# Kernel optimization log

Hardware: AMD Instinct MI355X
Metric: run time of the kernel (lower is better)

Reference implementation:

```python
import jax, jax.numpy as jnp
import numpy as np

N_HEAD = 8
DIM_K = 64
DIM_MODEL = N_HEAD * DIM_K  # 512; must equal seq_len for the final batch_dot
SCALE = DIM_K ** 0.5


def setup_inputs() -> dict:
    key = jax.random.key(0)
    ks = jax.random.split(key, 4)
    B, S, D_IN = 32, 512, 128
    x = jax.random.normal(ks[0], (B, S, D_IN), dtype=jnp.float32)
    init = 0.02
    Wq = jax.random.normal(ks[1], (D_IN * N_HEAD, DIM_MODEL), dtype=jnp.float32) * init
    Wk = jax.random.normal(ks[2], (D_IN * N_HEAD, DIM_MODEL), dtype=jnp.float32) * init
    Wv = jax.random.normal(ks[3], (D_IN * N_HEAD, DIM_MODEL), dtype=jnp.float32) * init
    z = jnp.zeros((DIM_MODEL,), dtype=jnp.float32)
    return {"x": x, "Wq": Wq, "bq": z, "Wk": Wk, "bk": z, "Wv": Wv, "bv": z}


def reference(x, Wq, bq, Wk, bk, Wv, bv):
    # Tile input n_head times along feature dim (matches K.concatenate([q]*n_head))
    xt = jnp.concatenate([x] * N_HEAD, axis=-1)          # [B, S, d_in*n_head]
    q = xt @ Wq + bq                                      # [B, S, dim_model]
    k = xt @ Wk + bk
    v = xt @ Wv + bv
    # K.batch_dot(q, k, axes=[-1,-1]) -> q @ k^T per batch
    scores = jnp.einsum('bsd,btd->bst', q, k) / SCALE     # [B, S, S]
    attn = jax.nn.softmax(scores, axis=-1)
    # K.batch_dot(v, attn, axes=[2,-1]): out[b,i,j] = sum_k v[b,i,k]*attn[b,j,k]
    # (only valid because S == dim_model, as in the original buggy layer)
    out = jnp.einsum('bik,bjk->bij', v, attn)             # [B, S, S]
    return out
```

## Files before the change

kernel.cpp:

```cpp
#include <hip/hip_runtime.h>


typedef unsigned short u16;
typedef __attribute__((ext_vector_type(8))) short bf16x8;
typedef __attribute__((ext_vector_type(4))) float f32x4;
typedef __attribute__((ext_vector_type(2))) float f32x2;

__device__ inline u16 f2bf(float f) {
  unsigned u = __float_as_uint(f);
  u = u + 0x7fffu + ((u >> 16) & 1u);
  return (u16)(u >> 16);
}
__device__ inline float bf2f(u16 h) { return __uint_as_float(((unsigned)h) << 16); }

__device__ inline void gl16(const u16* g, u16* l) {
  __builtin_amdgcn_global_load_lds(
      (const __attribute__((address_space(1))) unsigned int*)g,
      (__attribute__((address_space(3))) unsigned int*)l, 16, 0, 0);
}

__global__ __launch_bounds__(256)
void prep_w(const float* __restrict__ Wq, const float* __restrict__ Wk,
            const float* __restrict__ Wv,
            u16* __restrict__ WTh, u16* __restrict__ WTl) {
  __shared__ float sm[128][17];
  int t  = blockIdx.x >> 5;
  int nb = blockIdx.x & 31;
  const float* W = (t == 0) ? Wq : (t == 1) ? Wk : Wv;
  int n0 = nb << 4;
  int nl = threadIdx.x & 15;
  int kq = threadIdx.x >> 4;
  float s[8];
#pragma unroll
  for (int i = 0; i < 8; ++i) s[i] = 0.f;
#pragma unroll
  for (int h = 0; h < 8; ++h)
#pragma unroll
    for (int i = 0; i < 8; ++i)
      s[i] += W[(h * 128 + kq + (i << 4)) * 512 + n0 + nl];
#pragma unroll
  for (int i = 0; i < 8; ++i) sm[kq + (i << 4)][nl] = s[i];
  __syncthreads();
  int no = threadIdx.x >> 4;
  int k8 = (threadIdx.x & 15) << 3;
  bf16x8 h8, l8;
#pragma unroll
  for (int c = 0; c < 8; ++c) {
    float v = sm[k8 + c][no];
    u16 h = f2bf(v);
    h8[c] = (short)h;
    l8[c] = (short)f2bf(v - bf2f(h));
  }
  long o = (long)t * 65536 + (long)(n0 + no) * 128 + k8;
  *(bf16x8*)&WTh[o] = h8;
  *(bf16x8*)&WTl[o] = l8;
}

__global__ __launch_bounds__(256)
void split_x(const float* __restrict__ x, u16* __restrict__ xh, u16* __restrict__ xl) {
  int i = blockIdx.x * 256 + threadIdx.x;
  const f32x4* xx = (const f32x4*)x;
  f32x4 a = xx[i * 2], b = xx[i * 2 + 1];
  float v[8] = {a[0], a[1], a[2], a[3], b[0], b[1], b[2], b[3]};
  bf16x8 h8, l8;
#pragma unroll
  for (int j = 0; j < 8; ++j) {
    u16 h = f2bf(v[j]);
    h8[j] = (short)h;
    l8[j] = (short)f2bf(v[j] - bf2f(h));
  }
  ((bf16x8*)xh)[i] = h8;
  ((bf16x8*)xl)[i] = l8;
}

__global__ __launch_bounds__(256, 2)
void proj_fused(const u16* __restrict__ xh, const u16* __restrict__ xl,
                const u16* __restrict__ WTh, const u16* __restrict__ WTl,
                u16* __restrict__ Qh, u16* __restrict__ Kh, u16* __restrict__ Vh,
                const float* __restrict__ bq, const float* __restrict__ bk,
                const float* __restrict__ bv) {
  __shared__ __align__(16) char ldsraw[65536];
  u16* st = (u16*)ldsraw;

  int tid = threadIdx.x;
  int bid = blockIdx.x;
  bid = (bid & 7) * 192 + (bid >> 3);
  int which = bid % 3;
  int tile  = bid / 3;
  int mt = tile >> 2;
  int nt = tile & 3;

  const u16* Ah = xh + (long)mt * (128 * 128);
  const u16* Al = xl + (long)mt * (128 * 128);
  const u16* Bh = WTh + which * 65536 + nt * 16384;
  const u16* Bl = WTl + which * 65536 + nt * 16384;
  const float* bias = (which == 0) ? bq : (which == 1) ? bk : bv;
  u16* C = (which == 0) ? Qh : (which == 1) ? Kh : Vh;

  int lane = tid & 63;
  int wv = tid >> 6;
  int wm = (wv >> 1) << 6;
  int wn = (wv & 1) << 6;
  int frow = lane & 15;
  int fk = (lane >> 4) << 3;

  f32x4 acc[4][4];
#pragma unroll
  for (int i = 0; i < 4; ++i)
#pragma unroll
    for (int j = 0; j < 4; ++j) {
      f32x4 z = {0.f, 0.f, 0.f, 0.f};
      acc[i][j] = z;
    }

  for (int kk = 0; kk < 2; ++kk) {
    int k0 = kk << 6;
#pragma unroll
    for (int j = 0; j < 4; ++j) {
      int c = j * 256 + tid;
      int row = c >> 3;
      int scol = ((c & 7) ^ (row & 7)) << 3;
      int ga = row * 128 + k0 + scol;
      int lo = c << 3;
      gl16(Ah + ga, st + lo);
      gl16(Al + ga, st + 8192 + lo);
      gl16(Bh + ga, st + 16384 + lo);
      gl16(Bl + ga, st + 24576 + lo);
    }
    __syncthreads();
#pragma unroll
    for (int ks = 0; ks < 2; ++ks) {
      int kb = (ks << 5) + fk;
      bf16x8 a_h[4], a_l[4], b_h[4], b_l[4];
#pragma unroll
      for (int i = 0; i < 4; ++i) {
        int ar = wm + (i << 4) + frow;
        int ao = ar * 64 + (kb ^ ((ar & 7) << 3));
        a_h[i] = *(const bf16x8*)&st[ao];
        a_l[i] = *(const bf16x8*)&st[8192 + ao];
        int br = wn + (i << 4) + frow;
        int bo = br * 64 + (kb ^ ((br & 7) << 3));
        b_h[i] = *(const bf16x8*)&st[16384 + bo];
        b_l[i] = *(const bf16x8*)&st[24576 + bo];
      }
#pragma unroll
      for (int i = 0; i < 4; ++i)
#pragma unroll
        for (int j = 0; j < 4; ++j) {
          acc[i][j] = __builtin_amdgcn_mfma_f32_16x16x32_bf16(a_h[i], b_h[j], acc[i][j], 0, 0, 0);
          acc[i][j] = __builtin_amdgcn_mfma_f32_16x16x32_bf16(a_l[i], b_h[j], acc[i][j], 0, 0, 0);
          acc[i][j] = __builtin_amdgcn_mfma_f32_16x16x32_bf16(a_h[i], b_l[j], acc[i][j], 0, 0, 0);
        }
    }
    __syncthreads();
  }

  float* tr = ((float*)ldsraw) + wv * 2112;
  int lr = lane >> 3;
  int c8 = (lane & 7) << 3;
  int colbase = (nt << 7) + wn + c8;
  float bb[8];
#pragma unroll
  for (int c = 0; c < 8; ++c) bb[c] = bias[colbase + c];
  long rowg0 = (long)(mt << 7) + wm;
#pragma unroll
  for (int q = 0; q < 2; ++q) {
#pragma unroll
    for (int il = 0; il < 2; ++il) {
      int i = (q << 1) + il;
#pragma unroll
      for (int j = 0; j < 4; ++j)
#pragma unroll
        for (int r = 0; r < 4; ++r)
          tr[((il << 4) + ((lane >> 4) << 2) + r) * 66 + (j << 4) + (lane & 15)] =
              acc[i][j][r];
    }
#pragma unroll
    for (int p = 0; p < 4; ++p) {
      int rr = (p << 3) + lr;
      float v[8];
      *(f32x2*)&v[0] = *(const f32x2*)&tr[rr * 66 + c8];
      *(f32x2*)&v[2] = *(const f32x2*)&tr[rr * 66 + c8 + 2];
      *(f32x2*)&v[4] = *(const f32x2*)&tr[rr * 66 + c8 + 4];
      *(f32x2*)&v[6] = *(const f32x2*)&tr[rr * 66 + c8 + 6];
      bf16x8 o8;
#pragma unroll
      for (int c = 0; c < 8; ++c) o8[c] = (short)f2bf(v[c] + bb[c]);
      *(bf16x8*)&C[(rowg0 + (q << 5) + rr) * 512 + colbase] = o8;
    }
  }
}

__global__ __launch_bounds__(256, 4)
void nt_gemm1(const u16* __restrict__ A, const u16* __restrict__ B,
              float* __restrict__ C, float scale) {
  __shared__ __align__(16) u16 lds[2][128 * 64];
  int tid = threadIdx.x;
  int bid = blockIdx.x;
  bid = (bid & 7) * 64 + (bid >> 3);
  int b  = bid >> 4;
  int t  = bid & 15;
  int mt = t >> 2;
  int nt = t & 3;
  const u16* pA = A + (long)b * 262144 + (long)mt * (128 * 512);
  const u16* pB = B + (long)b * 262144 + (long)nt * (128 * 512);

  int lane = tid & 63;
  int wv = tid >> 6;
  int wm = (wv >> 1) << 6;
  int wn = (wv & 1) << 6;
  int frow = lane & 15;
  int fk = (lane >> 4) << 3;

  f32x4 acc[4][4];
#pragma unroll
  for (int i = 0; i < 4; ++i)
#pragma unroll
    for (int j = 0; j < 4; ++j) {
      f32x4 z = {0.f, 0.f, 0.f, 0.f};
      acc[i][j] = z;
    }

  for (int kk = 0; kk < 8; ++kk) {
    int k0 = kk << 6;
#pragma unroll
    for (int j = 0; j < 4; ++j) {
      int c = j * 256 + tid;
      int row = c >> 3;
      int scol = ((c & 7) ^ (row & 7)) << 3;
      long g = (long)row * 512 + k0 + scol;
      int lo = c << 3;
      gl16(pA + g, &lds[0][lo]);
      gl16(pB + g, &lds[1][lo]);
    }
    __syncthreads();
#pragma unroll
    for (int ks = 0; ks < 2; ++ks) {
      int kb = (ks << 5) + fk;
      bf16x8 av[4], bv_[4];
#pragma unroll
      for (int i = 0; i < 4; ++i) {
        int ar = wm + (i << 4) + frow;
        av[i] = *(const bf16x8*)&lds[0][ar * 64 + (kb ^ ((ar & 7) << 3))];
        int br = wn + (i << 4) + frow;
        bv_[i] = *(const bf16x8*)&lds[1][br * 64 + (kb ^ ((br & 7) << 3))];
      }
#pragma unroll
      for (int i = 0; i < 4; ++i)
#pragma unroll
        for (int j = 0; j < 4; ++j)
          acc[i][j] = __builtin_amdgcn_mfma_f32_16x16x32_bf16(av[i], bv_[j], acc[i][j], 0, 0, 0);
    }
    __syncthreads();
  }

  int rbase = (mt << 7) + wm + ((lane >> 4) << 2);
  int cbase = (nt << 7) + wn + (lane & 15);
  float* Cb = C + (long)b * 262144;
#pragma unroll
  for (int i = 0; i < 4; ++i)
#pragma unroll
    for (int j = 0; j < 4; ++j)
#pragma unroll
      for (int r = 0; r < 4; ++r)
        Cb[(long)(rbase + (i << 4) + r) * 512 + cbase + (j << 4)] = acc[i][j][r] * scale;
}

__global__ __launch_bounds__(256)
void softmax_rows(const float* __restrict__ S, u16* __restrict__ Ah) {
  int row  = (blockIdx.x << 2) + (threadIdx.x >> 6);
  int lane = threadIdx.x & 63;
  long base = (long)row * 512;
  const f32x4* s4 = (const f32x4*)(S + base);
  float v[8];
  *(f32x4*)&v[0] = s4[lane * 2];
  *(f32x4*)&v[4] = s4[lane * 2 + 1];
  float m = v[0];
#pragma unroll
  for (int j = 1; j < 8; ++j) m = fmaxf(m, v[j]);
#pragma unroll
  for (int o = 32; o > 0; o >>= 1) m = fmaxf(m, __shfl_xor(m, o));
  float sum = 0.f;
#pragma unroll
  for (int j = 0; j < 8; ++j) { v[j] = __expf(v[j] - m); sum += v[j]; }
#pragma unroll
  for (int o = 32; o > 0; o >>= 1) sum += __shfl_xor(sum, o);
  float inv = 1.f / sum;
  bf16x8 o8;
#pragma unroll
  for (int j = 0; j < 8; ++j) o8[j] = (short)f2bf(v[j] * inv);
  *(bf16x8*)&Ah[base + lane * 8] = o8;
}

extern "C" void kernel_launch(void* const* d_in, const int* in_sizes, int n_in,
                              void* d_out, int out_size, void* d_ws, size_t ws_size,
                              hipStream_t stream) {
  const float* x  = (const float*)d_in[0];
  const float* Wq = (const float*)d_in[1];
  const float* bq = (const float*)d_in[2];
  const float* Wk = (const float*)d_in[3];
  const float* bk = (const float*)d_in[4];
  const float* Wv = (const float*)d_in[5];
  const float* bv = (const float*)d_in[6];
  float* out = (float*)d_out;

  char* ws = (char*)d_ws;
  size_t off = 0;
  auto alloc = [&](size_t bytes) -> char* {
    char* p = ws + off;
    off = (off + bytes + 255) & ~(size_t)255;
    return p;
  };
  u16* WTh = (u16*)alloc((size_t)3 * 512 * 128 * 2);
  u16* WTl = (u16*)alloc((size_t)3 * 512 * 128 * 2);
  u16* xh  = (u16*)alloc((size_t)16384 * 128 * 2);
  u16* xl  = (u16*)alloc((size_t)16384 * 128 * 2);
  u16* Qh  = (u16*)alloc((size_t)16384 * 512 * 2);
  u16* Kh  = (u16*)alloc((size_t)16384 * 512 * 2);
  u16* Vh  = (u16*)alloc((size_t)16384 * 512 * 2);
  float* sc = (float*)alloc((size_t)32 * 512 * 512 * 4);
  u16* ah = Qh;

  prep_w<<<96, 256, 0, stream>>>(Wq, Wk, Wv, WTh, WTl);
  split_x<<<1024, 256, 0, stream>>>(x, xh, xl);
  proj_fused<<<1536, 256, 0, stream>>>(xh, xl, WTh, WTl, Qh, Kh, Vh, bq, bk, bv);
  nt_gemm1<<<512, 256, 0, stream>>>(Qh, Kh, sc, 0.125f);
  softmax_rows<<<4096, 256, 0, stream>>>(sc, ah);
  nt_gemm1<<<512, 256, 0, stream>>>(Vh, ah, out, 1.f);
}
```

Measured before the change: 92.92 us.

## Fuse QK^T, softmax and V·attn^T into one attention kernel per 64-row block

Replaces the scores GEMM, the separate softmax kernel and the second GEMM with one kernel. Each 512-thread block computes a 64x512 score tile, does the row softmax in registers with LDS reductions, keeps the bf16 probabilities in LDS, then multiplies by V. This removes the fp32 score round trip through global memory (32 MB written and read) and two kernel launches. In exchange it uses 128 KB of LDS, so only one block fits per CU, and the grid is just 256 blocks. K and V are also reloaded by each of the 8 row blocks per batch.

```diff
diff --git a/kernel.cpp b/kernel.cpp
--- a/kernel.cpp
+++ b/kernel.cpp
@@ -191,105 +191,219 @@
   }
 }
 
-__global__ __launch_bounds__(256, 4)
-void nt_gemm1(const u16* __restrict__ A, const u16* __restrict__ B,
-              float* __restrict__ C, float scale) {
-  __shared__ __align__(16) u16 lds[2][128 * 64];
+__global__ __launch_bounds__(512, 1)
+void attn_fused(const u16* __restrict__ Q, const u16* __restrict__ K,
+                const u16* __restrict__ V, float* __restrict__ OUT) {
+  __shared__ __align__(16) char LDS[131072];
+  u16* ldsQ = (u16*)LDS;
+  u16* ldsK = (u16*)(LDS + 8192);
+  u16* ldsV = (u16*)(LDS + 65536);
+  float* smax = (float*)(LDS + 73728);
+  float* ssum = (float*)(LDS + 74752);
+
   int tid = threadIdx.x;
   int bid = blockIdx.x;
-  bid = (bid & 7) * 64 + (bid >> 3);
-  int b  = bid >> 4;
-  int t  = bid & 15;
-  int mt = t >> 2;
-  int nt = t & 3;
-  const u16* pA = A + (long)b * 262144 + (long)mt * (128 * 512);
-  const u16* pB = B + (long)b * 262144 + (long)nt * (128 * 512);
+  bid = (bid & 7) * 32 + (bid >> 3);
+  int b  = bid >> 3;
+  int jb = bid & 7;
+
+  const u16* Qp = Q + ((long)b * 512 + jb * 64) * 512;
+  const u16* Kp = K + (long)b * 262144;
+  const u16* Vp = V + (long)b * 262144;
 
   int lane = tid & 63;
-  int wv = tid >> 6;
-  int wm = (wv >> 1) << 6;
-  int wn = (wv & 1) << 6;
+  int wv   = tid >> 6;
   int frow = lane & 15;
-  int fk = (lane >> 4) << 3;
-
-  f32x4 acc[4][4];
-#pragma unroll
-  for (int i = 0; i < 4; ++i)
-#pragma unroll
-    for (int j = 0; j < 4; ++j) {
+  int hi4  = lane >> 4;
+  int fk   = hi4 << 3;
+
+  int wm1 = (wv >> 2) << 5;
+  int wn1 = (wv & 3) << 7;
+  f32x4 acc[2][8];
+#pragma unroll
+  for (int i = 0; i < 2; ++i)
+#pragma unroll
+    for (int j = 0; j < 8; ++j) {
       f32x4 z = {0.f, 0.f, 0.f, 0.f};
       acc[i][j] = z;
     }
 
+  int qrow = tid >> 3, qcc = tid & 7;
+  int qscol = (qcc ^ (qrow & 7)) << 3;
   for (int kk = 0; kk < 8; ++kk) {
     int k0 = kk << 6;
-#pragma unroll
-    for (int j = 0; j < 4; ++j) {
-      int c = j * 256 + tid;
-      int row = c >> 3;
-      int scol = ((c & 7) ^ (row & 7)) << 3;
-      long g = (long)row * 512 + k0 + scol;
-      int lo = c << 3;
-      gl16(pA + g, &lds[0][lo]);
-      gl16(pB + g, &lds[1][lo]);
+    gl16(Qp + qrow * 512 + k0 + qscol, ldsQ + tid * 8);
+#pragma unroll
+    for (int j = 0; j < 8; ++j) {
+      int c = (j << 9) + tid;
+      int row = c >> 3, cc = c & 7;
+      int scol = (cc ^ (row & 7)) << 3;
+      gl16(Kp + (long)row * 512 + k0 + scol, ldsK + c * 8);
     }
     __syncthreads();
 #pragma unroll
     for (int ks = 0; ks < 2; ++ks) {
       int kb = (ks << 5) + fk;
-      bf16x8 av[4], bv_[4];
-#pragma unroll
-      for (int i = 0; i < 4; ++i) {
-        int ar = wm + (i << 4) + frow;
-        av[i] = *(const bf16x8*)&lds[0][ar * 64 + (kb ^ ((ar & 7) << 3))];
-        int br = wn + (i << 4) + frow;
-        bv_[i] = *(const bf16x8*)&lds[1][br * 64 + (kb ^ ((br & 7) << 3))];
-      }
-#pragma unroll
-      for (int i = 0; i < 4; ++i)
-#pragma unroll
-        for (int j = 0; j < 4; ++j)
-          acc[i][j] = __builtin_amdgcn_mfma_f32_16x16x32_bf16(av[i], bv_[j], acc[i][j], 0, 0, 0);
-    }
-    __syncthreads();
-  }
-
-  int rbase = (mt << 7) + wm + ((lane >> 4) << 2);
-  int cbase = (nt << 7) + wn + (lane & 15);
-  float* Cb = C + (long)b * 262144;
-#pragma unroll
-  for (int i = 0; i < 4; ++i)
-#pragma unroll
-    for (int j = 0; j < 4; ++j)
+      bf16x8 a[2], bb[8];
+#pragma unroll
+      for (int i = 0; i < 2; ++i) {
+        int ar = wm1 + (i << 4) + frow;
+        a[i] = *(const bf16x8*)&ldsQ[ar * 64 + (kb ^ ((ar & 7) << 3))];
+      }
+#pragma unroll
+      for (int j = 0; j < 8; ++j) {
+        int br = wn1 + (j << 4) + frow;
+        bb[j] = *(const bf16x8*)&ldsK[br * 64 + (kb ^ ((br & 7) << 3))];
+      }
+#pragma unroll
+      for (int i = 0; i < 2; ++i)
+#pragma unroll
+        for (int j = 0; j < 8; ++j)
+          acc[i][j] = __builtin_amdgcn_mfma_f32_16x16x32_bf16(a[i], bb[j], acc[i][j], 0, 0, 0);
+    }
+    __syncthreads();
+  }
+
+  float mx[2][4];
+#pragma unroll
+  for (int i = 0; i < 2; ++i)
+#pragma unroll
+    for (int r = 0; r < 4; ++r) {
+      float m = acc[i][0][r];
+#pragma unroll
+      for (int j = 1; j < 8; ++j) m = fmaxf(m, acc[i][j][r]);
+      mx[i][r] = m;
+    }
+#pragma unroll
+  for (int msk = 1; msk < 16; msk <<= 1)
+#pragma unroll
+    for (int i = 0; i < 2; ++i)
 #pragma unroll
       for (int r = 0; r < 4; ++r)
-        Cb[(long)(rbase + (i << 4) + r) * 512 + cbase + (j << 4)] = acc[i][j][r] * scale;
-}
-
-__global__ __launch_bounds__(256)
-void softmax_rows(const float* __restrict__ S, u16* __restrict__ Ah) {
-  int row  = (blockIdx.x << 2) + (threadIdx.x >> 6);
-  int lane = threadIdx.x & 63;
-  long base = (long)row * 512;
-  const f32x4* s4 = (const f32x4*)(S + base);
-  float v[8];
-  *(f32x4*)&v[0] = s4[lane * 2];
-  *(f32x4*)&v[4] = s4[lane * 2 + 1];
-  float m = v[0];
-#pragma unroll
-  for (int j = 1; j < 8; ++j) m = fmaxf(m, v[j]);
-#pragma unroll
-  for (int o = 32; o > 0; o >>= 1) m = fmaxf(m, __shfl_xor(m, o));
-  float sum = 0.f;
-#pragma unroll
-  for (int j = 0; j < 8; ++j) { v[j] = __expf(v[j] - m); sum += v[j]; }
-#pragma unroll
-  for (int o = 32; o > 0; o >>= 1) sum += __shfl_xor(sum, o);
-  float inv = 1.f / sum;
-  bf16x8 o8;
-#pragma unroll
-  for (int j = 0; j < 8; ++j) o8[j] = (short)f2bf(v[j] * inv);
-  *(bf16x8*)&Ah[base + lane * 8] = o8;
+        mx[i][r] = fmaxf(mx[i][r], __shfl_xor(mx[i][r], msk));
+  if (frow == 0) {
+#pragma unroll
+    for (int i = 0; i < 2; ++i)
+#pragma unroll
+      for (int r = 0; r < 4; ++r)
+        smax[(wm1 + (i << 4) + (hi4 << 2) + r) * 4 + (wv & 3)] = mx[i][r];
+  }
+  __syncthreads();
+  float mf[2][4];
+#pragma unroll
+  for (int i = 0; i < 2; ++i)
+#pragma unroll
+    for (int r = 0; r < 4; ++r) {
+      f32x4 mv = *(const f32x4*)&smax[(wm1 + (i << 4) + (hi4 << 2) + r) * 4];
+      mf[i][r] = fmaxf(fmaxf(mv[0], mv[1]), fmaxf(mv[2], mv[3]));
+    }
+  float sm[2][4];
+#pragma unroll
+  for (int i = 0; i < 2; ++i)
+#pragma unroll
+    for (int r = 0; r < 4; ++r) sm[i][r] = 0.f;
+#pragma unroll
+  for (int i = 0; i < 2; ++i)
+#pragma unroll
+    for (int j = 0; j < 8; ++j)
+#pragma unroll
+      for (int r = 0; r < 4; ++r) {
+        float p = __expf((acc[i][j][r] - mf[i][r]) * 0.125f);
+        acc[i][j][r] = p;
+        sm[i][r] += p;
+      }
+#pragma unroll
+  for (int msk = 1; msk < 16; msk <<= 1)
+#pragma unroll
+    for (int i = 0; i < 2; ++i)
+#pragma unroll
+      for (int r = 0; r < 4; ++r)
+        sm[i][r] += __shfl_xor(sm[i][r], msk);
+  if (frow == 0) {
+#pragma unroll
+    for (int i = 0; i < 2; ++i)
+#pragma unroll
+      for (int r = 0; r < 4; ++r)
+        ssum[(wm1 + (i << 4) + (hi4 << 2) + r) * 4 + (wv & 3)] = sm[i][r];
+  }
+  __syncthreads();
+  float inv[2][4];
+#pragma unroll
+  for (int i = 0; i < 2; ++i)
+#pragma unroll
+    for (int r = 0; r < 4; ++r) {
+      f32x4 sv = *(const f32x4*)&ssum[(wm1 + (i << 4) + (hi4 << 2) + r) * 4];
+      inv[i][r] = 1.f / (sv[0] + sv[1] + sv[2] + sv[3]);
+    }
+#pragma unroll
+  for (int i = 0; i < 2; ++i)
+#pragma unroll
+    for (int j = 0; j < 8; ++j)
+#pragma unroll
+      for (int r = 0; r < 4; ++r) {
+        int row = wm1 + (i << 4) + (hi4 << 2) + r;
+        int col = wn1 + (j << 4) + frow;
+        int byt = ((row << 10) + (col << 1)) ^ ((row & 7) << 4);
+        *(u16*)(LDS + byt) = f2bf(acc[i][j][r] * inv[i][r]);
+      }
+  __syncthreads();
+
+  int wm2 = (wv >> 1) << 7;
+  int wn2 = (wv & 1) << 5;
+  f32x4 a2[8][2];
+#pragma unroll
+  for (int i = 0; i < 8; ++i)
+#pragma unroll
+    for (int j = 0; j < 2; ++j) {
+      f32x4 z = {0.f, 0.f, 0.f, 0.f};
+      a2[i][j] = z;
+    }
+
+  for (int kk = 0; kk < 8; ++kk) {
+    int k0 = kk << 6;
+#pragma unroll
+    for (int j = 0; j < 8; ++j) {
+      int c = (j << 9) + tid;
+      int row = c >> 3, cc = c & 7;
+      int scol = (cc ^ (row & 7)) << 3;
+      gl16(Vp + (long)row * 512 + k0 + scol, ldsV + c * 8);
+    }
+    __syncthreads();
+#pragma unroll
+    for (int ks = 0; ks < 2; ++ks) {
+      int kb = (ks << 5) + fk;
+      bf16x8 a[8], bb[2];
+#pragma unroll
+      for (int i = 0; i < 8; ++i) {
+        int ar = wm2 + (i << 4) + frow;
+        a[i] = *(const bf16x8*)&ldsV[ar * 64 + (kb ^ ((ar & 7) << 3))];
+      }
+#pragma unroll
+      for (int j = 0; j < 2; ++j) {
+        int br = wn2 + (j << 4) + frow;
+        int byt = ((br << 10) + ((k0 + kb) << 1)) ^ ((br & 7) << 4);
+        bb[j] = *(const bf16x8*)(LDS + byt);
+      }
+#pragma unroll
+      for (int i = 0; i < 8; ++i)
+#pragma unroll
+        for (int j = 0; j < 2; ++j)
+          a2[i][j] = __builtin_amdgcn_mfma_f32_16x16x32_bf16(a[i], bb[j], a2[i][j], 0, 0, 0);
+    }
+    __syncthreads();
+  }
+
+  float* Ob = OUT + (long)b * 262144 + jb * 64;
+#pragma unroll
+  for (int i = 0; i < 8; ++i)
+#pragma unroll
+    for (int j = 0; j < 2; ++j)
+#pragma unroll
+      for (int r = 0; r < 4; ++r) {
+        int row = wm2 + (i << 4) + (hi4 << 2) + r;
+        int col = wn2 + (j << 4) + frow;
+        Ob[(long)row * 512 + col] = a2[i][j][r];
+      }
 }
 
 extern "C" void kernel_launch(void* const* d_in, const int* in_sizes, int n_in,
@@ -318,13 +432,9 @@
   u16* Qh  = (u16*)alloc((size_t)16384 * 512 * 2);
   u16* Kh  = (u16*)alloc((size_t)16384 * 512 * 2);
   u16* Vh  = (u16*)alloc((size_t)16384 * 512 * 2);
-  float* sc = (float*)alloc((size_t)32 * 512 * 512 * 4);
-  u16* ah = Qh;
 
   prep_w<<<96, 256, 0, stream>>>(Wq, Wk, Wv, WTh, WTl);
   split_x<<<1024, 256, 0, stream>>>(x, xh, xl);
   proj_fused<<<1536, 256, 0, stream>>>(xh, xl, WTh, WTl, Qh, Kh, Vh, bq, bk, bv);
-  nt_gemm1<<<512, 256, 0, stream>>>(Qh, Kh, sc, 0.125f);
-  softmax_rows<<<4096, 256, 0, stream>>>(sc, ah);
-  nt_gemm1<<<512, 256, 0, stream>>>(Vh, ah, out, 1.f);
-}
+  attn_fused<<<256, 512, 0, stream>>>(Qh, Kh, Vh, out);
+}
```

Result: faster. 87.24 us (-6.1%).

## Fuse QK^T, softmax, and V·P^T into a single attention kernel

Applied to the files above, without the earlier changes.

Replaces the scores GEMM, the separate row softmax kernel and the second GEMM with one kernel. Each block owns 32 query rows of one batch, keeps the full 32x512 score strip in registers, reduces max and sum across waves through LDS, and stores the normalized probabilities as bf16 in LDS for the second GEMM against staged V. This removes the fp32 score matrix round-trip to global memory and two launches. In exchange, the LDS footprint is large and occupancy drops to 2 blocks per CU, and each block re-reads the whole K and V for its batch.

```diff
diff --git a/kernel.cpp b/kernel.cpp
--- a/kernel.cpp
+++ b/kernel.cpp
@@ -5,6 +5,7 @@
 typedef __attribute__((ext_vector_type(8))) short bf16x8;
 typedef __attribute__((ext_vector_type(4))) float f32x4;
 typedef __attribute__((ext_vector_type(2))) float f32x2;
+typedef __attribute__((ext_vector_type(2))) unsigned int u32x2;
 
 __device__ inline u16 f2bf(float f) {
   unsigned u = __float_as_uint(f);
@@ -191,105 +192,199 @@
   }
 }
 
-__global__ __launch_bounds__(256, 4)
-void nt_gemm1(const u16* __restrict__ A, const u16* __restrict__ B,
-              float* __restrict__ C, float scale) {
-  __shared__ __align__(16) u16 lds[2][128 * 64];
+__global__ __launch_bounds__(256, 2)
+void attn_fused(const u16* __restrict__ Q, const u16* __restrict__ K,
+                const u16* __restrict__ V, float* __restrict__ OUT) {
+  __shared__ __align__(16) char LDS[67584];
+  u16* stg = (u16*)LDS;
+  u16* qt  = (u16*)(LDS + 32768);
+  float* smax = (float*)(LDS + 32768);
+  float* ssum = (float*)(LDS + 33280);
+  char* Pb = LDS + 34816;
+
   int tid = threadIdx.x;
-  int bid = blockIdx.x;
-  bid = (bid & 7) * 64 + (bid >> 3);
-  int b  = bid >> 4;
-  int t  = bid & 15;
-  int mt = t >> 2;
-  int nt = t & 3;
-  const u16* pA = A + (long)b * 262144 + (long)mt * (128 * 512);
-  const u16* pB = B + (long)b * 262144 + (long)nt * (128 * 512);
-
-  int lane = tid & 63;
-  int wv = tid >> 6;
-  int wm = (wv >> 1) << 6;
-  int wn = (wv & 1) << 6;
-  int frow = lane & 15;
-  int fk = (lane >> 4) << 3;
-
-  f32x4 acc[4][4];
-#pragma unroll
-  for (int i = 0; i < 4; ++i)
-#pragma unroll
-    for (int j = 0; j < 4; ++j) {
+  int p = blockIdx.x;
+  int xcd = p & 7, sq = p >> 3;
+  int b  = (xcd << 2) + (sq >> 4);
+  int jb = sq & 15;
+
+  const u16* Qp = Q + ((long)b * 512 + jb * 32) * 512;
+  const u16* Kp = K + (long)b * 262144;
+  const u16* Vp = V + (long)b * 262144;
+
+  int lane = tid & 63, nw = tid >> 6;
+  int frow = lane & 15, hi4 = lane >> 4;
+
+  auto stageKV = [&](const u16* src, int k0) {
+#pragma unroll
+    for (int j = 0; j < 8; ++j) {
+      int c = (j << 8) + tid;
+      int row = c >> 2, cc = c & 3;
+      int sc = (cc ^ ((row >> 1) & 3)) << 3;
+      gl16(src + (long)row * 512 + k0 + sc, stg + (c << 3));
+    }
+  };
+  auto stageQ = [&](int k0) {
+    if (tid < 128) {
+      int row = tid >> 2, cc = tid & 3;
+      int sc = (cc ^ ((row >> 1) & 3)) << 3;
+      gl16(Qp + (long)row * 512 + k0 + sc, qt + (tid << 3));
+    }
+  };
+
+  f32x4 acc[8][2];
+#pragma unroll
+  for (int j = 0; j < 8; ++j)
+#pragma unroll
+    for (int i = 0; i < 2; ++i) {
       f32x4 z = {0.f, 0.f, 0.f, 0.f};
-      acc[i][j] = z;
-    }
-
-  for (int kk = 0; kk < 8; ++kk) {
-    int k0 = kk << 6;
-#pragma unroll
-    for (int j = 0; j < 4; ++j) {
-      int c = j * 256 + tid;
-      int row = c >> 3;
-      int scol = ((c & 7) ^ (row & 7)) << 3;
-      long g = (long)row * 512 + k0 + scol;
-      int lo = c << 3;
-      gl16(pA + g, &lds[0][lo]);
-      gl16(pB + g, &lds[1][lo]);
-    }
+      acc[j][i] = z;
+    }
+
+  stageKV(Kp, 0);
+  stageQ(0);
+
+  for (int kk = 0; kk < 16; ++kk) {
     __syncthreads();
-#pragma unroll
-    for (int ks = 0; ks < 2; ++ks) {
-      int kb = (ks << 5) + fk;
-      bf16x8 av[4], bv_[4];
-#pragma unroll
-      for (int i = 0; i < 4; ++i) {
-        int ar = wm + (i << 4) + frow;
-        av[i] = *(const bf16x8*)&lds[0][ar * 64 + (kb ^ ((ar & 7) << 3))];
-        int br = wn + (i << 4) + frow;
-        bv_[i] = *(const bf16x8*)&lds[1][br * 64 + (kb ^ ((br & 7) << 3))];
+    bf16x8 a[8], bq_[2];
+#pragma unroll
+    for (int j = 0; j < 8; ++j) {
+      int R = (nw << 7) + (j << 4) + frow;
+      int cc = hi4 ^ ((R >> 1) & 3);
+      a[j] = *(const bf16x8*)&stg[(R << 5) + (cc << 3)];
+    }
+#pragma unroll
+    for (int i = 0; i < 2; ++i) {
+      int R = (i << 4) + frow;
+      int cc = hi4 ^ ((R >> 1) & 3);
+      bq_[i] = *(const bf16x8*)&qt[(R << 5) + (cc << 3)];
+    }
+    __syncthreads();
+    if (kk < 15) {
+      int k0 = (kk + 1) << 5;
+      stageKV(Kp, k0);
+      stageQ(k0);
+    } else {
+      stageKV(Vp, 0);
+    }
+#pragma unroll
+    for (int j = 0; j < 8; ++j)
+#pragma unroll
+      for (int i = 0; i < 2; ++i)
+        acc[j][i] = __builtin_amdgcn_mfma_f32_16x16x32_bf16(a[j], bq_[i], acc[j][i], 0, 0, 0);
+  }
+
+  float mx[2];
+#pragma unroll
+  for (int i = 0; i < 2; ++i) {
+    float m = acc[0][i][0];
+#pragma unroll
+    for (int j = 0; j < 8; ++j)
+#pragma unroll
+      for (int r = 0; r < 4; ++r) m = fmaxf(m, acc[j][i][r]);
+    m = fmaxf(m, __shfl_xor(m, 16));
+    m = fmaxf(m, __shfl_xor(m, 32));
+    mx[i] = m;
+  }
+  if (hi4 == 0) {
+#pragma unroll
+    for (int i = 0; i < 2; ++i) smax[(((i << 4) + frow) << 2) + nw] = mx[i];
+  }
+  __syncthreads();
+  float mf[2], sm_[2];
+#pragma unroll
+  for (int i = 0; i < 2; ++i) {
+    f32x4 m4 = *(const f32x4*)&smax[((i << 4) + frow) << 2];
+    mf[i] = fmaxf(fmaxf(m4[0], m4[1]), fmaxf(m4[2], m4[3]));
+    sm_[i] = 0.f;
+  }
+#pragma unroll
+  for (int j = 0; j < 8; ++j)
+#pragma unroll
+    for (int i = 0; i < 2; ++i)
+#pragma unroll
+      for (int r = 0; r < 4; ++r) {
+        float pv = __expf((acc[j][i][r] - mf[i]) * 0.125f);
+        acc[j][i][r] = pv;
+        sm_[i] += pv;
       }
 #pragma unroll
-      for (int i = 0; i < 4; ++i)
-#pragma unroll
-        for (int j = 0; j < 4; ++j)
-          acc[i][j] = __builtin_amdgcn_mfma_f32_16x16x32_bf16(av[i], bv_[j], acc[i][j], 0, 0, 0);
+  for (int i = 0; i < 2; ++i) {
+    sm_[i] += __shfl_xor(sm_[i], 16);
+    sm_[i] += __shfl_xor(sm_[i], 32);
+  }
+  if (hi4 == 0) {
+#pragma unroll
+    for (int i = 0; i < 2; ++i) ssum[(((i << 4) + frow) << 2) + nw] = sm_[i];
+  }
+  __syncthreads();
+  float inv_[2];
+#pragma unroll
+  for (int i = 0; i < 2; ++i) {
+    f32x4 s4 = *(const f32x4*)&ssum[((i << 4) + frow) << 2];
+    inv_[i] = 1.f / (s4[0] + s4[1] + s4[2] + s4[3]);
+  }
+#pragma unroll
+  for (int i = 0; i < 2; ++i) {
+    int qrow = (i << 4) + frow;
+#pragma unroll
+    for (int j = 0; j < 8; ++j) {
+      int col0 = (nw << 7) + (j << 4) + (hi4 << 2);
+      unsigned lo = (unsigned)f2bf(acc[j][i][0] * inv_[i]) |
+                    ((unsigned)f2bf(acc[j][i][1] * inv_[i]) << 16);
+      unsigned hi = (unsigned)f2bf(acc[j][i][2] * inv_[i]) |
+                    ((unsigned)f2bf(acc[j][i][3] * inv_[i]) << 16);
+      u32x2 w = {lo, hi};
+      int byt = ((qrow << 10) + (col0 << 1)) ^ ((qrow & 7) << 4);
+      *(u32x2*)(Pb + byt) = w;
+    }
+  }
+  __syncthreads();
+
+  f32x4 o[8][2];
+#pragma unroll
+  for (int j = 0; j < 8; ++j)
+#pragma unroll
+    for (int i = 0; i < 2; ++i) {
+      f32x4 z = {0.f, 0.f, 0.f, 0.f};
+      o[j][i] = z;
+    }
+
+  for (int kk = 0; kk < 16; ++kk) {
+    if (kk) __syncthreads();
+    int k0 = kk << 5;
+    bf16x8 av[8], bp[2];
+#pragma unroll
+    for (int j = 0; j < 8; ++j) {
+      int R = (nw << 7) + (j << 4) + frow;
+      int cc = hi4 ^ ((R >> 1) & 3);
+      av[j] = *(const bf16x8*)&stg[(R << 5) + (cc << 3)];
+    }
+#pragma unroll
+    for (int i = 0; i < 2; ++i) {
+      int R = (i << 4) + frow;
+      int byt = ((R << 10) + ((k0 + (hi4 << 3)) << 1)) ^ ((R & 7) << 4);
+      bp[i] = *(const bf16x8*)(Pb + byt);
     }
     __syncthreads();
-  }
-
-  int rbase = (mt << 7) + wm + ((lane >> 4) << 2);
-  int cbase = (nt << 7) + wn + (lane & 15);
-  float* Cb = C + (long)b * 262144;
-#pragma unroll
-  for (int i = 0; i < 4; ++i)
-#pragma unroll
-    for (int j = 0; j < 4; ++j)
-#pragma unroll
-      for (int r = 0; r < 4; ++r)
-        Cb[(long)(rbase + (i << 4) + r) * 512 + cbase + (j << 4)] = acc[i][j][r] * scale;
-}
-
-__global__ __launch_bounds__(256)
-void softmax_rows(const float* __restrict__ S, u16* __restrict__ Ah) {
-  int row  = (blockIdx.x << 2) + (threadIdx.x >> 6);
-  int lane = threadIdx.x & 63;
-  long base = (long)row * 512;
-  const f32x4* s4 = (const f32x4*)(S + base);
-  float v[8];
-  *(f32x4*)&v[0] = s4[lane * 2];
-  *(f32x4*)&v[4] = s4[lane * 2 + 1];
-  float m = v[0];
-#pragma unroll
-  for (int j = 1; j < 8; ++j) m = fmaxf(m, v[j]);
-#pragma unroll
-  for (int o = 32; o > 0; o >>= 1) m = fmaxf(m, __shfl_xor(m, o));
-  float sum = 0.f;
-#pragma unroll
-  for (int j = 0; j < 8; ++j) { v[j] = __expf(v[j] - m); sum += v[j]; }
-#pragma unroll
-  for (int o = 32; o > 0; o >>= 1) sum += __shfl_xor(sum, o);
-  float inv = 1.f / sum;
-  bf16x8 o8;
-#pragma unroll
-  for (int j = 0; j < 8; ++j) o8[j] = (short)f2bf(v[j] * inv);
-  *(bf16x8*)&Ah[base + lane * 8] = o8;
+    if (kk < 15) stageKV(Vp, (kk + 1) << 5);
+#pragma unroll
+    for (int j = 0; j < 8; ++j)
+#pragma unroll
+      for (int i = 0; i < 2; ++i)
+        o[j][i] = __builtin_amdgcn_mfma_f32_16x16x32_bf16(av[j], bp[i], o[j][i], 0, 0, 0);
+  }
+
+  float* Ob = OUT + (long)b * 262144 + jb * 32;
+#pragma unroll
+  for (int j = 0; j < 8; ++j)
+#pragma unroll
+    for (int i = 0; i < 2; ++i)
+#pragma unroll
+      for (int r = 0; r < 4; ++r) {
+        int vrow = (nw << 7) + (j << 4) + (hi4 << 2) + r;
+        Ob[(long)vrow * 512 + (i << 4) + frow] = o[j][i][r];
+      }
 }
 
 extern "C" void kernel_launch(void* const* d_in, const int* in_sizes, int n_in,
@@ -318,13 +413,9 @@
   u16* Qh  = (u16*)alloc((size_t)16384 * 512 * 2);
   u16* Kh  = (u16*)alloc((size_t)16384 * 512 * 2);
   u16* Vh  = (u16*)alloc((size_t)16384 * 512 * 2);
-  float* sc = (float*)alloc((size_t)32 * 512 * 512 * 4);
-  u16* ah = Qh;
 
   prep_w<<<96, 256, 0, stream>>>(Wq, Wk, Wv, WTh, WTl);
   split_x<<<1024, 256, 0, stream>>>(x, xh, xl);
   proj_fused<<<1536, 256, 0, stream>>>(xh, xl, WTh, WTl, Qh, Kh, Vh, bq, bk, bv);
-  nt_gemm1<<<512, 256, 0, stream>>>(Qh, Kh, sc, 0.125f);
-  softmax_rows<<<4096, 256, 0, stream>>>(sc, ah);
-  nt_gemm1<<<512, 256, 0, stream>>>(Vh, ah, out, 1.f);
-}
+  attn_fused<<<512, 256, 0, stream>>>(Qh, Kh, Vh, out);
+}
```

Measured after the change: 95.27 us. 2.5% more time.
